# Kernel optimization log

Measured on AMD Instinct MI355X. Metric: run time of the kernel, lower is better.

Reference implementation:

```python
import jax, jax.numpy as jnp
import numpy as np

# Architecture constants (from init_kwargs / ActionConfig)
R = 4          # vae_time_compression_ratio
WS = 2         # windows_size
PAD_T = R * WS # preprocessor left-padding
HID = 512      # action hidden_size
KD_IN = 16     # keyboard_dim_in (movement feature dim)
C_IMG = 3072   # img_hidden_size
KH = 1024      # keyboard_hidden_dim
NH = 16        # heads_num
HD = 64        # keyboard_head_dim
EPS = 1e-6


def setup_inputs() -> dict:
    key = jax.random.key(0)
    ks = jax.random.split(key, 8)
    B, T, Hs, Ws, NF = 1, 3, 44, 80, 81
    S = Hs * Ws

    def w(k, shape, s=0.02):
        return jax.random.normal(k, shape, jnp.float32) * s

    return {
        "x": jax.random.normal(ks[0], (B, T * S, C_IMG), jnp.float32),
        "condition": jax.random.normal(ks[1], (B, NF, KD_IN), jnp.float32),
        "me_w1": w(ks[2], (KD_IN, HID)), "me_b1": jnp.zeros((HID,), jnp.float32),
        "me_w2": w(ks[3], (HID, HID)), "me_b2": jnp.zeros((HID,), jnp.float32),
        "q_w": w(ks[4], (C_IMG, KH)), "q_b": jnp.zeros((KH,), jnp.float32),
        "kv_w": w(ks[5], (HID * WS * R, 2 * KH)), "kv_b": jnp.zeros((2 * KH,), jnp.float32),
        "qn_w": jnp.ones((HD,), jnp.float32), "kn_w": jnp.ones((HD,), jnp.float32),
        "out_w": w(ks[6], (KH, C_IMG)), "out_b": jnp.zeros((C_IMG,), jnp.float32),
        "H": Hs, "W": Ws, "T": T, "num_frame_per_block": T,
    }


def _rmsnorm(x, w):
    return x * jax.lax.rsqrt(jnp.mean(x * x, axis=-1, keepdims=True) + EPS) * w


def _preprocess(condition, me_w1, me_b1, me_w2, me_b2, num_frame_per_block):
    # MovementPreprocessor.forward with is_causal=True
    B, NF, _ = condition.shape
    pad = jnp.broadcast_to(condition[:, :1, :], (B, PAD_T, condition.shape[-1]))
    cp = jnp.concatenate([pad, condition], axis=1)            # [B, PAD_T+NF, KD_IN]
    emb = jax.nn.silu(cp @ me_w1 + me_b1) @ me_w2 + me_b2     # [B, PAD_T+NF, HID]
    n_feats = (NF - 1) // R + 1
    start = R * (n_feats - num_frame_per_block - WS) + PAD_T  # python int (static)
    emb = emb[:, start:, :]
    # vectorized replacement of the python-loop window slicing+stack
    win = jnp.arange(num_frame_per_block)[:, None] * R + jnp.arange(WS * R)[None, :]
    gm = emb[:, win, :]                                       # [B, L, WS*R, HID]
    return gm.reshape(B, num_frame_per_block, WS * R * HID)   # [B, L, 4096]


def reference(x, condition, me_w1, me_b1, me_w2, me_b2, q_w, q_b, kv_w, kv_b,
              qn_w, kn_w, out_w, out_b, H, W, T, num_frame_per_block):
    B = x.shape[0]
    S = H * W
    L = num_frame_per_block

    mf = _preprocess(condition, me_w1, me_b1, me_w2, me_b2, L)  # [B, L, HID*WS*R]

    # q: [B, T*S, C_IMG] -> [B, S, T, h, d]
    q = (x @ q_w + q_b).reshape(B, T, S, NH, HD).transpose(0, 2, 1, 3, 4)

    # k, v: [B, L, h, d] (NOT expanded over S; broadcast inside attention instead)
    kv = (mf @ kv_w + kv_b).reshape(B, L, 2, NH, HD)
    k, v = kv[:, :, 0], kv[:, :, 1]

    q = _rmsnorm(q, qn_w)
    k = _rmsnorm(k, kn_w)

    scale = 1.0 / np.sqrt(HD).astype(np.float32)
    scores = jnp.einsum('bsthd,blhd->bshtl', q, k) * scale      # [B,S,h,T,L]
    attn = jax.nn.softmax(scores, axis=-1)
    o = jnp.einsum('bshtl,blhd->bsthd', attn, v)                # [B,S,T,h,d]

    # '(B S) T H D -> B (T S) (H D)'
    o = o.transpose(0, 2, 1, 3, 4).reshape(B, T * S, NH * HD)
    return x + (o @ out_w + out_b)
```

## Files before the change

### kernel.cpp

```cpp
#include <hip/hip_runtime.h>

#define TOK  10560
#define CIMG 3072
#define KHD  1024

typedef unsigned short ushort_t;
typedef unsigned int u32;
using bf16x8 = __attribute__((ext_vector_type(8))) __bf16;
using f32x4  = __attribute__((ext_vector_type(4))) float;

#define GLD_LDS16(gp, lp) __builtin_amdgcn_global_load_lds( \
    (const __attribute__((address_space(1))) u32*)(gp), \
    (__attribute__((address_space(3))) u32*)(lp), 16, 0, 0)

static __device__ __forceinline__ unsigned short f2bf(float f){
  union { float f; unsigned u; } x; x.f = f;
  unsigned r = x.u + 0x7fffu + ((x.u >> 16) & 1u);
  return (unsigned short)(r >> 16);
}
static __device__ __forceinline__ float wave_sum(float v){
  #pragma unroll
  for (int off = 32; off > 0; off >>= 1) v += __shfl_xor(v, off, 64);
  return v;
}

__global__ __launch_bounds__(256) void k_pre1(const float* __restrict__ cond,
    const float* __restrict__ w1, const float* __restrict__ b1,
    float* __restrict__ h1){
  __shared__ float cs[16][16];
  int t = threadIdx.x;
  if (t < 256) cs[t >> 4][t & 15] = cond[(64 + (t >> 4)) * 16 + (t & 15)];
  __syncthreads();
  #pragma unroll
  for (int i = 0; i < 4; ++i){
    int idx = blockIdx.x * 256 + t + i * 2048;
    int r = idx >> 9, c = idx & 511;
    float s = b1[c];
    #pragma unroll
    for (int j = 0; j < 16; ++j) s += cs[r][j] * w1[j * 512 + c];
    h1[idx] = s / (1.f + __expf(-s));
  }
}

__global__ __launch_bounds__(256) void k_pre2(const float* __restrict__ h1,
    const float* __restrict__ w2, const float* __restrict__ b2,
    float* __restrict__ emb){
  int idx = blockIdx.x * 256 + threadIdx.x;
  int r = idx >> 9, c = idx & 511;
  const float* hp = h1 + r * 512;
  const float* wp = w2 + c;
  float acc = b2[c];
  #pragma unroll 8
  for (int j = 0; j < 512; ++j) acc += hp[j] * wp[(size_t)j * 512];
  emb[idx] = acc;
}

__global__ __launch_bounds__(256) void k_kv(const float* __restrict__ emb,
                                            const float* __restrict__ kvw,
                                            float* __restrict__ part){
  int bl = blockIdx.x;
  int l = bl / 128, rem = bl % 128, nt = rem / 16, kc = rem % 16;
  int n = nt * 256 + threadIdx.x;
  const float* e = emb + 2048 * l + kc * 256;
  const float* w = kvw + (size_t)(kc * 256) * 2048 + n;
  float acc = 0.f;
  for (int r = 0; r < 256; ++r) acc += e[r] * w[(size_t)r * 2048];
  part[kc * 6144 + l * 2048 + n] = acc;
}

__global__ void k_knorm(const float* __restrict__ part, const float* __restrict__ kvb,
                        const float* __restrict__ knw, float* __restrict__ kn,
                        float* __restrict__ vv){
  int wid = threadIdx.x >> 6, lane = threadIdx.x & 63;
  for (int i = 0; i < 12; ++i){
    int g = wid * 12 + i;
    int l = g >> 4, h = g & 15;
    int ik = l * 2048 + h * 64 + lane;
    float kk = kvb[h * 64 + lane];
    float v  = kvb[1024 + h * 64 + lane];
    for (int p = 0; p < 16; ++p){ kk += part[p * 6144 + ik]; v += part[p * 6144 + ik + 1024]; }
    float ss = wave_sum(kk * kk);
    kn[l * 1024 + h * 64 + lane] = kk * rsqrtf(ss * (1.f/64.f) + 1e-6f) * knw[lane];
    vv[l * 1024 + h * 64 + lane] = v;
  }
}

__global__ __launch_bounds__(256) void k_tconv(const float* __restrict__ src,
                                               ushort_t* __restrict__ dst,
                                               int R, int C){
  __shared__ float tile[32][33];
  int nTr = R >> 5;
  int tr = blockIdx.x % nTr, tc = blockIdx.x / nTr;
  int r0 = tr * 32, c0 = tc * 32, t = threadIdx.x;
  #pragma unroll
  for (int i = 0; i < 4; ++i){
    int idx = t + i * 256; int r = idx >> 5, c = idx & 31;
    tile[r][c] = src[(size_t)(r0 + r) * C + c0 + c];
  }
  __syncthreads();
  #pragma unroll
  for (int i = 0; i < 4; ++i){
    int idx = t + i * 256; int rr = idx >> 5, cc = idx & 31;
    dst[(size_t)(c0 + rr) * R + r0 + cc] = f2bf(tile[cc][rr]);
  }
}

__global__ __launch_bounds__(256) void k_xconv(const float* __restrict__ x,
                                               ushort_t* __restrict__ xb, int n4){
  for (int i = blockIdx.x * 256 + threadIdx.x; i < n4; i += gridDim.x * 256){
    float4 v = ((const float4*)x)[i];
    ushort4 o;
    o.x = f2bf(v.x); o.y = f2bf(v.y); o.z = f2bf(v.z); o.w = f2bf(v.w);
    ((ushort4*)xb)[i] = o;
  }
}

__global__ __launch_bounds__(512, 2) void gemm_fused(
    const ushort_t* __restrict__ A, const ushort_t* __restrict__ Bt,
    int Mdim, int Kdim, int Ndim,
    const float* __restrict__ bias, const float* __restrict__ kn,
    const float* __restrict__ qnw, float* __restrict__ acoef){
  __shared__ __align__(16) unsigned char lds[131072];
  const int tid = threadIdx.x;
  const int lane = tid & 63, wid = tid >> 6;
  const int wm = wid >> 2, wn = wid & 3;
  const int l15 = lane & 15, kg = lane >> 4;
  const int ntiles = Ndim >> 8;

  int bid = blockIdx.x;
  const int cpx = gridDim.x >> 3;
  bid = (bid & 7) * cpx + (bid >> 3);
  const int mt = bid / ntiles, nt = bid % ntiles;
  const int mbase = mt << 8, nbase = nt << 8;

  const int sr  = tid >> 1;
  const int skh = (tid & 1) ^ ((sr >> 2) & 1);
  int arow = mbase + sr; if (arow >= Mdim) arow = Mdim - 1;
  const ushort_t* gA = A  + (size_t)arow * Kdim + skh * 8;
  const ushort_t* gB = Bt + (size_t)(nbase + sr) * Kdim + skh * 8;
  const int wofs = wid * 1024;

  auto stage = [&](int t, int c, int b){
    const int gk = t * 64 + c * 16;
    unsigned char* dst = lds + b * 65536 + c * 8192 + wofs;
    GLD_LDS16(gA + gk, dst);
    GLD_LDS16(gB + gk, dst + 32768);
  };

  const int arl = wm * 128 + l15;
  const int brl = wn * 64 + l15;
  const int kh  = ((kg & 1) ^ ((l15 >> 2) & 1)) * 16;
  const unsigned aBase = (unsigned)((kg >> 1) * 8192 + arl * 32 + kh);
  const unsigned bBase = (unsigned)(32768 + (kg >> 1) * 8192 + brl * 32 + kh);

  f32x4 acc[8][4];
  #pragma unroll
  for (int m = 0; m < 8; ++m)
    #pragma unroll
    for (int n = 0; n < 4; ++n) acc[m][n] = {0.f, 0.f, 0.f, 0.f};

  bf16x8 afr[4], bfr[4];

#define PH_READ_B(base, KSL) { _Pragma("unroll") \
    for (int n = 0; n < 4; ++n) \
      bfr[n] = *(const bf16x8*)((base) + bBase + (KSL)*16384 + n*512); }
#define PH_READ_A(base, KSL, M0) { _Pragma("unroll") \
    for (int m = 0; m < 4; ++m) \
      afr[m] = *(const bf16x8*)((base) + aBase + (KSL)*16384 + ((M0)+m)*512); }
#define PH_MFMA(R0) { __builtin_amdgcn_s_setprio(1); _Pragma("unroll") \
    for (int m = 0; m < 4; ++m){ _Pragma("unroll") \
      for (int n = 0; n < 4; ++n) \
        acc[(R0)+m][n] = __builtin_amdgcn_mfma_f32_16x16x32_bf16(afr[m], bfr[n], acc[(R0)+m][n], 0, 0, 0); } \
    __builtin_amdgcn_s_setprio(0); }

  const int T = Kdim >> 6;

  stage(0, 0, 0); stage(0, 1, 0); stage(0, 2, 0); stage(0, 3, 0);
  asm volatile("s_waitcnt vmcnt(4)" ::: "memory");
  __builtin_amdgcn_s_barrier();

  for (int t = 0; t < T - 1; ++t){
    const int b = t & 1;
    const unsigned char* base = lds + b * 65536;
    PH_READ_B(base, 0); PH_READ_A(base, 0, 0);
    stage(t + 1, 0, b ^ 1);
    __builtin_amdgcn_s_barrier();
    PH_MFMA(0);
    __builtin_amdgcn_s_barrier();
    PH_READ_A(base, 0, 4);
    stage(t + 1, 1, b ^ 1);
    asm volatile("s_waitcnt vmcnt(4)" ::: "memory");
    __builtin_amdgcn_s_barrier();
    PH_MFMA(4);
    __builtin_amdgcn_s_barrier();
    PH_READ_B(base, 1); PH_READ_A(base, 1, 0);
    stage(t + 1, 2, b ^ 1);
    __builtin_amdgcn_s_barrier();
    PH_MFMA(0);
    __builtin_amdgcn_s_barrier();
    PH_READ_A(base, 1, 4);
    stage(t + 1, 3, b ^ 1);
    asm volatile("s_waitcnt vmcnt(4)" ::: "memory");
    __builtin_amdgcn_s_barrier();
    PH_MFMA(4);
    __builtin_amdgcn_s_barrier();
  }
  {
    const unsigned char* base = lds + ((T - 1) & 1) * 65536;
    PH_READ_B(base, 0); PH_READ_A(base, 0, 0);
    __builtin_amdgcn_s_barrier();
    PH_MFMA(0);
    __builtin_amdgcn_s_barrier();
    PH_READ_A(base, 0, 4);
    asm volatile("s_waitcnt vmcnt(0)" ::: "memory");
    __builtin_amdgcn_s_barrier();
    PH_MFMA(4);
    __builtin_amdgcn_s_barrier();
    PH_READ_B(base, 1); PH_READ_A(base, 1, 0);
    PH_MFMA(0);
    PH_READ_A(base, 1, 4);
    PH_MFMA(4);
  }
#undef PH_READ_B
#undef PH_READ_A
#undef PH_MFMA

  const int hglob = nt * 4 + wn;
  float qnwv[4], qbv[4], knv0[4], knv1[4], knv2[4];
  #pragma unroll
  for (int n = 0; n < 4; ++n){
    int d = n * 16 + l15;
    qnwv[n] = qnw[d];
    qbv[n]  = bias[nbase + wn * 64 + d];
    knv0[n] = kn[hglob * 64 + d];
    knv1[n] = kn[1024 + hglob * 64 + d];
    knv2[n] = kn[2048 + hglob * 64 + d];
  }
  #pragma unroll
  for (int m = 0; m < 8; ++m){
    #pragma unroll
    for (int j = 0; j < 4; ++j){
      float q[4], ssq = 0.f;
      #pragma unroll
      for (int n = 0; n < 4; ++n){ q[n] = acc[m][n][j] + qbv[n]; ssq += q[n] * q[n]; }
      #pragma unroll
      for (int off = 1; off < 16; off <<= 1) ssq += __shfl_xor(ssq, off, 64);
      float rs = rsqrtf(ssq * (1.f/64.f) + 1e-6f);
      float s0 = 0.f, s1 = 0.f, s2 = 0.f;
      #pragma unroll
      for (int n = 0; n < 4; ++n){
        float qn = q[n] * rs * qnwv[n];
        s0 += qn * knv0[n]; s1 += qn * knv1[n]; s2 += qn * knv2[n];
      }
      #pragma unroll
      for (int off = 1; off < 16; off <<= 1){
        s0 += __shfl_xor(s0, off, 64);
        s1 += __shfl_xor(s1, off, 64);
        s2 += __shfl_xor(s2, off, 64);
      }
      s0 *= 0.125f; s1 *= 0.125f; s2 *= 0.125f;
      float mx = fmaxf(s0, fmaxf(s1, s2));
      float e0 = __expf(s0 - mx), e1 = __expf(s1 - mx), e2 = __expf(s2 - mx);
      float inv = 1.f / (e0 + e1 + e2);
      int grow = mbase + wm * 128 + m * 16 + kg * 4 + j;
      if (l15 == 0 && grow < Mdim){
        float2 a12 = {e1 * inv, e2 * inv};
        *(float2*)(acoef + (size_t)grow * 32 + hglob * 2) = a12;
      }
    }
  }
}

__global__ __launch_bounds__(512) void k_uv(const float* __restrict__ vv,
    const float* __restrict__ ow, float* __restrict__ U){
  int b = blockIdx.x;
  int i = b / 6, cc = b % 6;
  int h = i / 3, l = i % 3;
  int c = cc * 512 + threadIdx.x;
  const float* vp = vv + l * 1024 + h * 64;
  const float* wp = ow + (size_t)(h * 64) * 3072 + c;
  float acc = 0.f;
  #pragma unroll
  for (int d = 0; d < 64; ++d) acc += vp[d] * wp[(size_t)d * 3072];
  U[(size_t)i * 3072 + c] = acc;
}

__global__ __launch_bounds__(256) void k_ubase(const float* __restrict__ U,
    const float* __restrict__ ob, float* __restrict__ base, float* __restrict__ D){
  int c = blockIdx.x * 256 + threadIdx.x;
  float b = ob[c];
  #pragma unroll
  for (int h = 0; h < 16; ++h){
    float u0 = U[(size_t)(h * 3 + 0) * 3072 + c];
    float u1 = U[(size_t)(h * 3 + 1) * 3072 + c];
    float u2 = U[(size_t)(h * 3 + 2) * 3072 + c];
    b += u0;
    D[(size_t)(h * 2 + 0) * 3072 + c] = u1 - u0;
    D[(size_t)(h * 2 + 1) * 3072 + c] = u2 - u0;
  }
  base[c] = b;
}

__global__ __launch_bounds__(256) void k_rank32(const float* __restrict__ x,
    const float* __restrict__ acoef, const float* __restrict__ D,
    const float* __restrict__ base, float* __restrict__ out){
  const int tid = threadIdx.x;
  const int cc = blockIdx.x % 6, ms = blockIdx.x / 6;
  const int c = cc * 512 + tid * 2;
  const int t0 = ms * 120;

  float ur0[32], ur1[32];
  #pragma unroll
  for (int i = 0; i < 32; ++i){
    float2 d2 = *(const float2*)(D + (size_t)i * 3072 + c);
    ur0[i] = d2.x; ur1[i] = d2.y;
  }
  float2 b2 = *(const float2*)(base + c);
  const float* ap = acoef + (size_t)t0 * 32;

  #pragma unroll 2
  for (int r = 0; r < 120; ++r){
    const size_t o = (size_t)(t0 + r) * 3072 + c;
    float2 xv = *(const float2*)(x + o);
    float a0 = 0.f, a1 = 0.f;
    #pragma unroll
    for (int k = 0; k < 32; ++k){
      float av = ap[r * 32 + k];
      a0 += av * ur0[k];
      a1 += av * ur1[k];
    }
    float2 ov = {xv.x + b2.x + a0, xv.y + b2.y + a1};
    *(float2*)(out + o) = ov;
  }
}

extern "C" void kernel_launch(void* const* d_in, const int* in_sizes, int n_in,
                              void* d_out, int out_size, void* d_ws, size_t ws_size,
                              hipStream_t stream){
  const float* x    = (const float*)d_in[0];
  const float* cond = (const float*)d_in[1];
  const float* mew1 = (const float*)d_in[2];
  const float* meb1 = (const float*)d_in[3];
  const float* mew2 = (const float*)d_in[4];
  const float* meb2 = (const float*)d_in[5];
  const float* qw   = (const float*)d_in[6];
  const float* qb   = (const float*)d_in[7];
  const float* kvw  = (const float*)d_in[8];
  const float* kvb  = (const float*)d_in[9];
  const float* qnw  = (const float*)d_in[10];
  const float* knw  = (const float*)d_in[11];
  const float* ow   = (const float*)d_in[12];
  const float* ob   = (const float*)d_in[13];

  char* ws = (char*)d_ws;
  float*    emb    = (float*)(ws + 0);
  float*    kvpart = (float*)(ws + 32768);
  float*    kn     = (float*)(ws + 425984);
  float*    vv     = (float*)(ws + 438272);
  ushort_t* qwt    = (ushort_t*)(ws + 450560);
  float*    U      = (float*)(ws + 6742016);
  float*    base   = (float*)(ws + 7331840);
  float*    Dbuf   = (float*)(ws + 7344128);
  float*    acoef  = (float*)(ws + 7737344);
  float*    h1buf  = (float*)(ws + 9089024);

  ushort_t* xb = (ushort_t*)d_out;

  k_pre1<<<8, 256, 0, stream>>>(cond, mew1, meb1, h1buf);
  k_pre2<<<32, 256, 0, stream>>>(h1buf, mew2, meb2, emb);
  k_kv<<<384, 256, 0, stream>>>(emb, kvw, kvpart);
  k_knorm<<<1, 256, 0, stream>>>(kvpart, kvb, knw, kn, vv);
  k_uv<<<288, 512, 0, stream>>>(vv, ow, U);
  k_ubase<<<12, 256, 0, stream>>>(U, ob, base, Dbuf);
  k_tconv<<<3072, 256, 0, stream>>>(qw, qwt, 3072, 1024);
  k_xconv<<<2048, 256, 0, stream>>>(x, xb, (TOK * CIMG) / 4);
  gemm_fused<<<42 * 4, 512, 0, stream>>>(xb, qwt, TOK, CIMG, KHD, qb, kn, qnw, acoef);
  k_rank32<<<88 * 6, 256, 0, stream>>>(x, acoef, Dbuf, base, (float*)d_out);
}
```

Baseline: 310.1 us.

## Retile Q GEMM to 192x128 blocks and compute rank-32 output via MFMA

The Q-projection GEMM moves from 256x256 tiles (168 blocks) to 192x128 tiles (440 blocks). It uses less LDS and allows higher occupancy, and six waves now load A while two load B. The attention coefficients and the D matrix are stored as bf16, with D transposed, so the final rank-32 update plus residual can run as a single 16x16x32 bf16 MFMA per tile instead of scalar FMAs. The aim is better CU utilization on the GEMM and a cheaper epilogue kernel, at the cost of reduced precision in the rank-32 correction and a simpler K-loop pipeline with fewer overlap phases.

```diff
diff --git a/kernel.cpp b/kernel.cpp
--- a/kernel.cpp
+++ b/kernel.cpp
@@ -115,117 +115,106 @@
   }
 }
 
-__global__ __launch_bounds__(512, 2) void gemm_fused(
+__global__ __launch_bounds__(512, 4) void gemm_fused(
     const ushort_t* __restrict__ A, const ushort_t* __restrict__ Bt,
-    int Mdim, int Kdim, int Ndim,
     const float* __restrict__ bias, const float* __restrict__ kn,
-    const float* __restrict__ qnw, float* __restrict__ acoef){
-  __shared__ __align__(16) unsigned char lds[131072];
+    const float* __restrict__ qnw, u32* __restrict__ acoefb){
+  __shared__ __align__(16) unsigned char lds[81920];
   const int tid = threadIdx.x;
   const int lane = tid & 63, wid = tid >> 6;
-  const int wm = wid >> 2, wn = wid & 3;
+  const int wm = wid >> 1, wn = wid & 1;
   const int l15 = lane & 15, kg = lane >> 4;
-  const int ntiles = Ndim >> 8;
 
   int bid = blockIdx.x;
-  const int cpx = gridDim.x >> 3;
-  bid = (bid & 7) * cpx + (bid >> 3);
-  const int mt = bid / ntiles, nt = bid % ntiles;
-  const int mbase = mt << 8, nbase = nt << 8;
+  bid = (bid & 7) * 55 + (bid >> 3);
+  const int mt = bid >> 3, nt = bid & 7;
+  const int mbase = mt * 192, nbase = nt << 7;
 
   const int sr  = tid >> 1;
   const int skh = (tid & 1) ^ ((sr >> 2) & 1);
-  int arow = mbase + sr; if (arow >= Mdim) arow = Mdim - 1;
-  const ushort_t* gA = A  + (size_t)arow * Kdim + skh * 8;
-  const ushort_t* gB = Bt + (size_t)(nbase + sr) * Kdim + skh * 8;
-  const int wofs = wid * 1024;
+  const ushort_t* gA = A + (size_t)(mbase + sr) * CIMG + skh * 8;
+  const int u   = tid - 384;
+  const int skb = (u & 1) ^ ((u >> 3) & 1);
+  const ushort_t* gB0 = Bt + (size_t)(nbase + (u >> 1)) * CIMG + skb * 8;
+  const ushort_t* gB1 = gB0 + (size_t)64 * CIMG;
 
   auto stage = [&](int t, int c, int b){
     const int gk = t * 64 + c * 16;
-    unsigned char* dst = lds + b * 65536 + c * 8192 + wofs;
-    GLD_LDS16(gA + gk, dst);
-    GLD_LDS16(gB + gk, dst + 32768);
+    if (wid < 6){
+      unsigned char* dst = lds + b * 40960 + c * 6144 + wid * 1024;
+      GLD_LDS16(gA + gk, dst);
+    } else {
+      unsigned char* dst = lds + b * 40960 + 24576 + c * 4096 + (wid - 6) * 1024;
+      GLD_LDS16(gB0 + gk, dst);
+      GLD_LDS16(gB1 + gk, dst + 2048);
+    }
   };
-
-  const int arl = wm * 128 + l15;
+#define WAITC2 { if (wid < 6) asm volatile("s_waitcnt vmcnt(2)" ::: "memory"); \
+                 else         asm volatile("s_waitcnt vmcnt(4)" ::: "memory"); }
+
+  const int arl = wm * 48 + l15;
   const int brl = wn * 64 + l15;
   const int kh  = ((kg & 1) ^ ((l15 >> 2) & 1)) * 16;
-  const unsigned aBase = (unsigned)((kg >> 1) * 8192 + arl * 32 + kh);
-  const unsigned bBase = (unsigned)(32768 + (kg >> 1) * 8192 + brl * 32 + kh);
-
-  f32x4 acc[8][4];
-  #pragma unroll
-  for (int m = 0; m < 8; ++m)
+  const unsigned aBase = (unsigned)((kg >> 1) * 6144 + arl * 32 + kh);
+  const unsigned bBase = (unsigned)(24576 + (kg >> 1) * 4096 + brl * 32 + kh);
+
+  f32x4 acc[3][4];
+  #pragma unroll
+  for (int m = 0; m < 3; ++m)
     #pragma unroll
     for (int n = 0; n < 4; ++n) acc[m][n] = {0.f, 0.f, 0.f, 0.f};
 
-  bf16x8 afr[4], bfr[4];
-
-#define PH_READ_B(base, KSL) { _Pragma("unroll") \
+  bf16x8 afr[3], bfr[4];
+
+#define PH_READ(base, KSL) { _Pragma("unroll") \
     for (int n = 0; n < 4; ++n) \
-      bfr[n] = *(const bf16x8*)((base) + bBase + (KSL)*16384 + n*512); }
-#define PH_READ_A(base, KSL, M0) { _Pragma("unroll") \
-    for (int m = 0; m < 4; ++m) \
-      afr[m] = *(const bf16x8*)((base) + aBase + (KSL)*16384 + ((M0)+m)*512); }
-#define PH_MFMA(R0) { __builtin_amdgcn_s_setprio(1); _Pragma("unroll") \
-    for (int m = 0; m < 4; ++m){ _Pragma("unroll") \
+      bfr[n] = *(const bf16x8*)((base) + bBase + (KSL)*8192 + n*512); \
+    _Pragma("unroll") \
+    for (int m = 0; m < 3; ++m) \
+      afr[m] = *(const bf16x8*)((base) + aBase + (KSL)*12288 + m*512); }
+#define PH_MFMA { __builtin_amdgcn_s_setprio(1); _Pragma("unroll") \
+    for (int m = 0; m < 3; ++m){ _Pragma("unroll") \
       for (int n = 0; n < 4; ++n) \
-        acc[(R0)+m][n] = __builtin_amdgcn_mfma_f32_16x16x32_bf16(afr[m], bfr[n], acc[(R0)+m][n], 0, 0, 0); } \
+        acc[m][n] = __builtin_amdgcn_mfma_f32_16x16x32_bf16(afr[m], bfr[n], acc[m][n], 0, 0, 0); } \
     __builtin_amdgcn_s_setprio(0); }
 
-  const int T = Kdim >> 6;
+  const int T = CIMG / 64;
 
   stage(0, 0, 0); stage(0, 1, 0); stage(0, 2, 0); stage(0, 3, 0);
-  asm volatile("s_waitcnt vmcnt(4)" ::: "memory");
+  WAITC2;
   __builtin_amdgcn_s_barrier();
 
   for (int t = 0; t < T - 1; ++t){
     const int b = t & 1;
-    const unsigned char* base = lds + b * 65536;
-    PH_READ_B(base, 0); PH_READ_A(base, 0, 0);
-    stage(t + 1, 0, b ^ 1);
-    __builtin_amdgcn_s_barrier();
-    PH_MFMA(0);
-    __builtin_amdgcn_s_barrier();
-    PH_READ_A(base, 0, 4);
-    stage(t + 1, 1, b ^ 1);
-    asm volatile("s_waitcnt vmcnt(4)" ::: "memory");
-    __builtin_amdgcn_s_barrier();
-    PH_MFMA(4);
-    __builtin_amdgcn_s_barrier();
-    PH_READ_B(base, 1); PH_READ_A(base, 1, 0);
-    stage(t + 1, 2, b ^ 1);
-    __builtin_amdgcn_s_barrier();
-    PH_MFMA(0);
-    __builtin_amdgcn_s_barrier();
-    PH_READ_A(base, 1, 4);
-    stage(t + 1, 3, b ^ 1);
-    asm volatile("s_waitcnt vmcnt(4)" ::: "memory");
-    __builtin_amdgcn_s_barrier();
-    PH_MFMA(4);
+    const unsigned char* base = lds + b * 40960;
+    PH_READ(base, 0);
+    stage(t + 1, 0, b ^ 1); stage(t + 1, 1, b ^ 1);
+    WAITC2;
+    __builtin_amdgcn_s_barrier();
+    PH_MFMA;
+    __builtin_amdgcn_s_barrier();
+    PH_READ(base, 1);
+    stage(t + 1, 2, b ^ 1); stage(t + 1, 3, b ^ 1);
+    WAITC2;
+    __builtin_amdgcn_s_barrier();
+    PH_MFMA;
     __builtin_amdgcn_s_barrier();
   }
   {
-    const unsigned char* base = lds + ((T - 1) & 1) * 65536;
-    PH_READ_B(base, 0); PH_READ_A(base, 0, 0);
-    __builtin_amdgcn_s_barrier();
-    PH_MFMA(0);
-    __builtin_amdgcn_s_barrier();
-    PH_READ_A(base, 0, 4);
+    const unsigned char* base = lds + ((T - 1) & 1) * 40960;
+    PH_READ(base, 0);
     asm volatile("s_waitcnt vmcnt(0)" ::: "memory");
     __builtin_amdgcn_s_barrier();
-    PH_MFMA(4);
-    __builtin_amdgcn_s_barrier();
-    PH_READ_B(base, 1); PH_READ_A(base, 1, 0);
-    PH_MFMA(0);
-    PH_READ_A(base, 1, 4);
-    PH_MFMA(4);
-  }
-#undef PH_READ_B
-#undef PH_READ_A
+    PH_MFMA;
+    __builtin_amdgcn_s_barrier();
+    PH_READ(base, 1);
+    PH_MFMA;
+  }
+#undef PH_READ
 #undef PH_MFMA
-
-  const int hglob = nt * 4 + wn;
+#undef WAITC2
+
+  const int hglob = nt * 2 + wn;
   float qnwv[4], qbv[4], knv0[4], knv1[4], knv2[4];
   #pragma unroll
   for (int n = 0; n < 4; ++n){
@@ -237,7 +226,7 @@
     knv2[n] = kn[2048 + hglob * 64 + d];
   }
   #pragma unroll
-  for (int m = 0; m < 8; ++m){
+  for (int m = 0; m < 3; ++m){
     #pragma unroll
     for (int j = 0; j < 4; ++j){
       float q[4], ssq = 0.f;
@@ -262,10 +251,10 @@
       float mx = fmaxf(s0, fmaxf(s1, s2));
       float e0 = __expf(s0 - mx), e1 = __expf(s1 - mx), e2 = __expf(s2 - mx);
       float inv = 1.f / (e0 + e1 + e2);
-      int grow = mbase + wm * 128 + m * 16 + kg * 4 + j;
-      if (l15 == 0 && grow < Mdim){
-        float2 a12 = {e1 * inv, e2 * inv};
-        *(float2*)(acoef + (size_t)grow * 32 + hglob * 2) = a12;
+      int grow = mbase + wm * 48 + m * 16 + kg * 4 + j;
+      if (l15 == 0){
+        u32 pk = (u32)f2bf(e1 * inv) | ((u32)f2bf(e2 * inv) << 16);
+        acoefb[(size_t)grow * 16 + hglob] = pk;
       }
     }
   }
@@ -286,7 +275,8 @@
 }
 
 __global__ __launch_bounds__(256) void k_ubase(const float* __restrict__ U,
-    const float* __restrict__ ob, float* __restrict__ base, float* __restrict__ D){
+    const float* __restrict__ ob, float* __restrict__ base,
+    ushort_t* __restrict__ Dt){
   int c = blockIdx.x * 256 + threadIdx.x;
   float b = ob[c];
   #pragma unroll
@@ -295,42 +285,34 @@
     float u1 = U[(size_t)(h * 3 + 1) * 3072 + c];
     float u2 = U[(size_t)(h * 3 + 2) * 3072 + c];
     b += u0;
-    D[(size_t)(h * 2 + 0) * 3072 + c] = u1 - u0;
-    D[(size_t)(h * 2 + 1) * 3072 + c] = u2 - u0;
+    Dt[(size_t)c * 32 + h * 2 + 0] = f2bf(u1 - u0);
+    Dt[(size_t)c * 32 + h * 2 + 1] = f2bf(u2 - u0);
   }
   base[c] = b;
 }
 
-__global__ __launch_bounds__(256) void k_rank32(const float* __restrict__ x,
-    const float* __restrict__ acoef, const float* __restrict__ D,
+__global__ __launch_bounds__(256) void k_rankmm(const float* __restrict__ x,
+    const ushort_t* __restrict__ ab, const ushort_t* __restrict__ Dt,
     const float* __restrict__ base, float* __restrict__ out){
   const int tid = threadIdx.x;
-  const int cc = blockIdx.x % 6, ms = blockIdx.x / 6;
-  const int c = cc * 512 + tid * 2;
-  const int t0 = ms * 120;
-
-  float ur0[32], ur1[32];
-  #pragma unroll
-  for (int i = 0; i < 32; ++i){
-    float2 d2 = *(const float2*)(D + (size_t)i * 3072 + c);
-    ur0[i] = d2.x; ur1[i] = d2.y;
-  }
-  float2 b2 = *(const float2*)(base + c);
-  const float* ap = acoef + (size_t)t0 * 32;
-
-  #pragma unroll 2
-  for (int r = 0; r < 120; ++r){
-    const size_t o = (size_t)(t0 + r) * 3072 + c;
-    float2 xv = *(const float2*)(x + o);
-    float a0 = 0.f, a1 = 0.f;
+  const int wid = tid >> 6, lane = tid & 63;
+  const int l15 = lane & 15, kg = lane >> 4;
+  const int rtile = blockIdx.x / 6, cc = blockIdx.x % 6;
+  const int row0 = rtile * 64 + wid * 16;
+  const int col0 = cc * 512;
+  bf16x8 afr = *(const bf16x8*)(ab + (size_t)(row0 + l15) * 32 + kg * 8);
+  #pragma unroll 4
+  for (int ct = 0; ct < 32; ++ct){
+    int col = col0 + ct * 16 + l15;
+    bf16x8 bfr = *(const bf16x8*)(Dt + (size_t)col * 32 + kg * 8);
+    f32x4 acc = {0.f, 0.f, 0.f, 0.f};
+    acc = __builtin_amdgcn_mfma_f32_16x16x32_bf16(afr, bfr, acc, 0, 0, 0);
+    float bs = base[col];
     #pragma unroll
-    for (int k = 0; k < 32; ++k){
-      float av = ap[r * 32 + k];
-      a0 += av * ur0[k];
-      a1 += av * ur1[k];
+    for (int j = 0; j < 4; ++j){
+      size_t o = (size_t)(row0 + kg * 4 + j) * 3072 + col;
+      out[o] = x[o] + bs + acc[j];
     }
-    float2 ov = {xv.x + b2.x + a0, xv.y + b2.y + a1};
-    *(float2*)(out + o) = ov;
   }
 }
 
@@ -360,9 +342,9 @@
   ushort_t* qwt    = (ushort_t*)(ws + 450560);
   float*    U      = (float*)(ws + 6742016);
   float*    base   = (float*)(ws + 7331840);
-  float*    Dbuf   = (float*)(ws + 7344128);
-  float*    acoef  = (float*)(ws + 7737344);
-  float*    h1buf  = (float*)(ws + 9089024);
+  ushort_t* Dt     = (ushort_t*)(ws + 7344128);
+  u32*      acoefb = (u32*)(ws + 7540736);
+  float*    h1buf  = (float*)(ws + 8216576);
 
   ushort_t* xb = (ushort_t*)d_out;
 
@@ -371,9 +353,9 @@
   k_kv<<<384, 256, 0, stream>>>(emb, kvw, kvpart);
   k_knorm<<<1, 256, 0, stream>>>(kvpart, kvb, knw, kn, vv);
   k_uv<<<288, 512, 0, stream>>>(vv, ow, U);
-  k_ubase<<<12, 256, 0, stream>>>(U, ob, base, Dbuf);
+  k_ubase<<<12, 256, 0, stream>>>(U, ob, base, Dt);
   k_tconv<<<3072, 256, 0, stream>>>(qw, qwt, 3072, 1024);
   k_xconv<<<2048, 256, 0, stream>>>(x, xb, (TOK * CIMG) / 4);
-  gemm_fused<<<42 * 4, 512, 0, stream>>>(xb, qwt, TOK, CIMG, KHD, qb, kn, qnw, acoef);
-  k_rank32<<<88 * 6, 256, 0, stream>>>(x, acoef, Dbuf, base, (float*)d_out);
-}
+  gemm_fused<<<440, 512, 0, stream>>>(xb, qwt, qb, kn, qnw, acoefb);
+  k_rankmm<<<990, 256, 0, stream>>>(x, (const ushort_t*)acoefb, Dt, base, (float*)d_out);
+}
```

After: 307.4 us. Within noise of the previous version (-0.9%).
